# Performance work log

Measured on AMD Instinct MI355X. Metric: run time of the kernel, lower is better.

## Reference

```python
import jax, jax.numpy as jnp
import numpy as np

N_COUPLES = 16      # 32 frames / tubelet-depth 2
GRID = 14           # 224 / 16 patches per row
CUBE = 9            # 729 = 9^3
VOL = (N_COUPLES * CUBE, GRID * CUBE, GRID * CUBE)  # (144, 126, 126)
OUT = (64, 64, 64)


def _nearest_idx(out_size, in_size):
    # torch F.interpolate(mode='nearest'): src = floor(dst * in/out)
    return jnp.floor(jnp.arange(out_size) * (in_size / out_size)).astype(jnp.int32)


def setup_inputs() -> dict:
    key = jax.random.key(0)
    hidden_states = jax.random.normal(key, (64, 3137, 768), dtype=jnp.float32)
    return {"hidden_states": hidden_states}


def reference(hidden_states) -> jnp.ndarray:
    B = hidden_states.shape[0]
    # drop CLS token -> [B, 3136, 768]
    x = hidden_states[:, 1:, :]
    # 1D nearest resize 768 -> 729 along feature dim
    x = x[:, :, _nearest_idx(CUBE ** 3, x.shape[-1])]  # [B, 3136, 729]
    # reverse_patching, fully vectorized:
    # token (couple i, row r, col p) with cube (d0,d1,d2) -> volume[9i+d0, 9r+d1, 9p+d2]
    v = x.reshape(B, N_COUPLES, GRID, GRID, CUBE, CUBE, CUBE)
    v = v.transpose(0, 1, 4, 2, 5, 3, 6).reshape(B, *VOL)  # [B, 144, 126, 126]
    # 3D nearest resize (144,126,126) -> (64,64,64)
    i0 = _nearest_idx(OUT[0], VOL[0])
    i1 = _nearest_idx(OUT[1], VOL[1])
    i2 = _nearest_idx(OUT[2], VOL[2])
    out = v[:, i0][:, :, i1][:, :, :, i2]  # [B, 64, 64, 64]
    return out[:, None]  # [B, 1, 64, 64, 64]
```

## Files before the change

kernel.cpp:

```cpp
#include <hip/hip_runtime.h>
#include <hip/hip_bf16.h>


#define TOKENS 3137
#define CHANNELS 768

__global__ __launch_bounds__(256) void gather4_kernel(const float* __restrict__ in,
                                                      float* __restrict__ out) {
    const float ch_scale = (float)(768.0 / 729.0);

    int gid = blockIdx.x * 256 + threadIdx.x;
    int o2 = gid & 63;
    int r  = gid >> 6;
    int o1 = r & 63;
    r >>= 6;
    int q  = r & 15;
    int b  = r >> 4;

    int i0 = (q  * 144) >> 6;
    int i1 = (o1 * 126) >> 6;
    int i2 = (o2 * 126) >> 6;

    int nq = i0 / 9, c0 = i0 - nq * 9;
    int g1 = i1 / 9, c1 = i1 - g1 * 9;
    int g2 = i2 / 9, c2 = i2 - g2 * 9;

    int cc = (c0 * 9 + c1) * 9 + c2;
    int ch = (int)floorf((float)cc * ch_scale);

    int t = 1 + (nq * 14 + g1) * 14 + g2;

    const float* src = in + ((long long)(b * TOKENS + t) * CHANNELS + ch);
    float v0 = src[0];
    float v1 = src[1 * 784 * CHANNELS];
    float v2 = src[2 * 784 * CHANNELS];
    float v3 = src[3 * 784 * CHANNELS];

    float* dst = out + ((((b << 6) | q) << 6 | o1) << 6 | o2);
    dst[0 << 16] = v0;
    dst[1 << 16] = v1;
    dst[2 << 16] = v2;
    dst[3 << 16] = v3;
}

extern "C" void kernel_launch(void* const* d_in, const int* in_sizes, int n_in,
                              void* d_out, int out_size, void* d_ws, size_t ws_size,
                              hipStream_t stream) {
    const float* in = (const float*)d_in[0];
    float* out = (float*)d_out;
    int blocks = 4194304 / 256;
    gather4_kernel<<<blocks, 256, 0, stream>>>(in, out);
}
```

Before: 82.00 us.

## Stage needed channel bands per token row in LDS with float4 loads

Each block now handles one (batch, couple, patch-row) group. It loads only the channel bands that the output actually samples for the 14 tokens into shared memory, using coalesced float4 loads, then writes outputs from LDS. This replaces scattered per-element global gathers, which fetched whole cache lines for single floats. The cost is a sync per block, hand-derived band offsets that must match the nearest-index maths, and fewer blocks.

```diff
diff --git a/kernel.cpp b/kernel.cpp
--- a/kernel.cpp
+++ b/kernel.cpp
@@ -4,43 +4,65 @@
 
 #define TOKENS 3137
 #define CHANNELS 768
+#define BANDW 92
+#define TOKSTRIDE 372
 
-__global__ __launch_bounds__(256) void gather4_kernel(const float* __restrict__ in,
-                                                      float* __restrict__ out) {
+__global__ __launch_bounds__(256) void gather_lds_kernel(const float* __restrict__ in,
+                                                         float* __restrict__ out) {
     const float ch_scale = (float)(768.0 / 729.0);
+    __shared__ float lds[14 * TOKSTRIDE];
 
-    int gid = blockIdx.x * 256 + threadIdx.x;
-    int o2 = gid & 63;
-    int r  = gid >> 6;
-    int o1 = r & 63;
-    r >>= 6;
-    int q  = r & 15;
+    int bx = blockIdx.x;
+    int g1 = bx % 14;
+    int r  = bx / 14;
+    int n  = r & 15;
     int b  = r >> 4;
 
-    int i0 = (q  * 144) >> 6;
-    int i1 = (o1 * 126) >> 6;
-    int i2 = (o2 * 126) >> 6;
+    int tid = threadIdx.x;
+    int tbase = 1 + (n * 14 + g1) * 14;
+    long long rowbase = (long long)(b * TOKENS + tbase) * CHANNELS;
 
-    int nq = i0 / 9, c0 = i0 - nq * 9;
-    int g1 = i1 / 9, c1 = i1 - g1 * 9;
-    int g2 = i2 / 9, c2 = i2 - g2 * 9;
+    float4* lds4 = (float4*)lds;
+    for (int idx = tid; idx < 14 * 93; idx += 256) {
+        int g2 = idx / 93;
+        int r2 = idx - 93 * g2;
+        if (r2 < 92) {
+            int band  = r2 / 23;
+            int chunk = r2 - 23 * band;
+            int bb = 170 * band - 2 * (band & 1);
+            const float4* src =
+                (const float4*)(in + rowbase + (long long)g2 * CHANNELS + bb);
+            lds4[idx] = src[chunk];
+        }
+    }
+    __syncthreads();
 
-    int cc = (c0 * 9 + c1) * 9 + c2;
-    int ch = (int)floorf((float)cc * ch_scale);
+    int o2 = tid & 63;
+    int i2 = (o2 * 63) >> 5;
+    int g2 = i2 / 9;
+    int c2 = i2 - 9 * g2;
+    int lane_o1 = tid >> 6;
 
-    int t = 1 + (nq * 14 + g1) * 14 + g2;
+    int o1s  = (32 * g1 + 6) / 7;
+    int cnt1 = (32 * (g1 + 1) + 6) / 7 - o1s;
 
-    const float* src = in + ((long long)(b * TOKENS + t) * CHANNELS + ch);
-    float v0 = src[0];
-    float v1 = src[1 * 784 * CHANNELS];
-    float v2 = src[2 * 784 * CHANNELS];
-    float v3 = src[3 * 784 * CHANNELS];
+    const float* ldsg2 = lds + g2 * TOKSTRIDE;
 
-    float* dst = out + ((((b << 6) | q) << 6 | o1) << 6 | o2);
-    dst[0 << 16] = v0;
-    dst[1 << 16] = v1;
-    dst[2 << 16] = v2;
-    dst[3 << 16] = v3;
+    for (int o0loc = 0; o0loc < 4; ++o0loc) {
+        int bb = 170 * o0loc - 2 * (o0loc & 1);
+        int ccb = 162 * o0loc;
+        const float* ldsrow = ldsg2 + o0loc * BANDW - bb;
+        int o0 = 4 * n + o0loc;
+        for (int o1loc = lane_o1; o1loc < cnt1; o1loc += 4) {
+            int o1 = o1s + o1loc;
+            int i1 = (o1 * 63) >> 5;
+            int c1 = i1 - 9 * g1;
+            int cc = ccb + c1 * 9 + c2;
+            int ch = (int)floorf((float)cc * ch_scale);
+            float v = ldsrow[ch];
+            out[(((b * 64 + o0) * 64 + o1) << 6) | o2] = v;
+        }
+    }
 }
 
 extern "C" void kernel_launch(void* const* d_in, const int* in_sizes, int n_in,
@@ -48,6 +70,6 @@
                               hipStream_t stream) {
     const float* in = (const float*)d_in[0];
     float* out = (float*)d_out;
-    int blocks = 4194304 / 256;
-    gather4_kernel<<<blocks, 256, 0, stream>>>(in, out);
+    int blocks = 64 * 16 * 14;
+    gather_lds_kernel<<<blocks, 256, 0, stream>>>(in, out);
 }
```

Result: slower. 96.63 us (+17.8%).
